# Kernel optimization log

Measured on AMD Instinct MI355X. Metric: run time of the kernel, lower is better.

## Reference

```python
import jax, jax.numpy as jnp
import numpy as np

HEADS = 8
GS = 16
C = 512
E = 512
SCALE = (E / HEADS) ** -0.5
PNAMES = ['sa_qkv_w','sa_qkv_b','sa_pa_w','sa_pa_b','sa_ln1_g','sa_ln1_b','sa_f1_w','sa_f1_b','sa_f2_w','sa_f2_b','sa_ln2_g','sa_ln2_b','sa_c1_w','sa_c1_b','sa_c2_w','sa_c2_b','sa_bn_g','sa_bn_b','ca_q_w','ca_q_b','ca_k_w','ca_k_b','ca_v_w','ca_v_b','ca_pa_w','ca_pa_b','p_q_w','p_q_b','p_k_w','p_k_b','p_v_w','p_v_b','p_pa_w','p_pa_b','p_ln_g','p_ln_b','p_lin_w','p_lin_b']


def _ln(x, g, b, eps=1e-5):
    m = x.mean(-1, keepdims=True)
    v = jnp.var(x, axis=-1, keepdims=True)
    return (x - m) / jnp.sqrt(v + eps) * g + b


def _conv1x1(x, w, b):
    return jnp.einsum('bchw,oc->bohw', x, w) + b[None, :, None, None]


def _up_ac(x, out=GS):
    # bilinear upsample, align_corners=True (nn.UpsamplingBilinear2d)
    H = x.shape[2]
    pos = jnp.arange(out) * (H - 1) / (out - 1)
    lo = jnp.floor(pos).astype(jnp.int32)
    hi = jnp.minimum(lo + 1, H - 1)
    w = (pos - lo).astype(x.dtype)
    xr = x[:, :, lo, :] * (1 - w)[None, None, :, None] + x[:, :, hi, :] * w[None, None, :, None]
    return xr[:, :, :, lo] * (1 - w) + xr[:, :, :, hi] * w


def _asri(x, p):
    # Sequence_ASRI: GAP tokens -> attention over the batch axis -> pixel-shuffle back
    B = x.shape[0]; ch = E // HEADS
    gap = x.mean((2, 3))                                             # [B,C]
    qkv = (gap @ p['sa_qkv_w'].T + p['sa_qkv_b']).reshape(B, 4, ch, HEADS).transpose(1, 3, 0, 2)  # [4,H,B,ch]
    q, k, v, skip = qkv[0], qkv[1], qkv[2], qkv[3]
    attn = jax.nn.softmax(jnp.einsum('hbc,hdc->hbd', q, k) * SCALE, -1)  # [H,B,B]
    o = jnp.einsum('hbd,hdc->hbc', attn, v)
    merge = lambda t: t.transpose(1, 2, 0).reshape(B, E)             # 'head b c -> b (c head)'
    a = merge(o) @ p['sa_pa_w'].T + p['sa_pa_b'] + merge(skip)
    h = jax.nn.relu(_ln(a, p['sa_ln1_g'], p['sa_ln1_b']) @ p['sa_f1_w'].T + p['sa_f1_b'])
    a = h @ p['sa_f2_w'].T + p['sa_f2_b'] + a
    s = _ln(a, p['sa_ln2_g'], p['sa_ln2_b']) @ p['sa_c1_w'].T + p['sa_c1_b']  # [B,C*16]
    s = _up_ac(s.reshape(B, C, 4, 4))                                 # pixel shuffle p1=p2=4 then bilinear to 16x16
    s = _conv1x1(s, p['sa_c2_w'], p['sa_c2_b'])
    # BatchNorm2d in eval mode (running_mean=0, running_var=1, eps=1e-5)
    s = s / np.float32(np.sqrt(1.0 + 1e-5)) * p['sa_bn_g'][None, :, None, None] + p['sa_bn_b'][None, :, None, None]
    return x + jax.nn.relu(s)


def _sscm(x1, x2, p):
    # Sequence_SSCM: GAP-token q/k over batch axis, full spatial v
    B = x1.shape[0]; ch = E // HEADS
    q = (x1.mean((2, 3)) @ p['ca_q_w'].T + p['ca_q_b']).reshape(B, ch, HEADS).transpose(2, 0, 1)  # [H,B,ch]
    k = (x2.mean((2, 3)) @ p['ca_k_w'].T + p['ca_k_b']).reshape(B, ch, HEADS).transpose(2, 0, 1)
    v = _conv1x1(x2, p['ca_v_w'], p['ca_v_b']).reshape(B, ch, HEADS, GS, GS).transpose(2, 0, 1, 3, 4).reshape(HEADS, B, ch * GS * GS)
    attn = jax.nn.softmax(jnp.einsum('hbc,hdc->hbd', q, k) * SCALE, -1)  # [H,B,B]
    o = jnp.einsum('hbd,hdm->hbm', attn, v)
    o = o.reshape(HEADS, B, ch, GS, GS).transpose(1, 2, 0, 3, 4).reshape(B, E, GS, GS)
    return jax.nn.relu(_conv1x1(o, p['ca_pa_w'], p['ca_pa_b']))


def _pixel(x1, x2, p):
    # Pixel_SSCM: pixel-wise cross-batch attention (no scale -- matches source)
    B = x1.shape[0]; ch = E // HEADS; N = GS * GS
    split = lambda t: t.reshape(B, ch, HEADS, N).transpose(2, 0, 3, 1)   # 'b (c head) h w -> head b (h w) c'
    q = split(_conv1x1(x1, p['p_q_w'], p['p_q_b']))                      # [H,B,N,ch]
    k = split(_conv1x1(x2, p['p_k_w'], p['p_k_b']))
    v = split(_conv1x1(x2, p['p_v_w'], p['p_v_b'])).reshape(HEADS, B * N, ch)
    attn = jax.nn.softmax(jnp.einsum('hbnc,hqmc->hbqnm', q, k), -1)      # [H,B,B,N,N]
    attn = attn.transpose(1, 0, 3, 2, 4).reshape(B, HEADS, N, B * N)     # 'head b q h w -> b head h (q w)'
    o = jnp.einsum('bhnm,hmc->bhnc', attn, v)
    o = o.transpose(0, 3, 1, 2).reshape(B, E, GS, GS)                    # 'b head (h w) c -> b (c head) h w'
    o = _conv1x1(o, p['p_pa_w'], p['p_pa_b']) + x1
    t = o.reshape(B, C, N).transpose(0, 2, 1)                            # [B,N,C]
    t = jax.nn.relu(_ln(t, p['p_ln_g'], p['p_ln_b']) @ p['p_lin_w'].T + p['p_lin_b'])
    return t.transpose(0, 2, 1).reshape(B, C, GS, GS)


def _hrlm(p, xs, xq):
    sa_s = _asri(xs, p)
    sa_q = _asri(xq, p)
    ca_s = _sscm(sa_s, sa_q, p)
    ca_q = _sscm(sa_q, sa_s, p)
    return _pixel(sa_s, ca_q, p), _pixel(sa_q, ca_s, p)


def setup_inputs():
    key = jax.random.key(0)
    ks = iter(jax.random.split(key, 64))
    w = lambda *s: (jax.random.normal(next(ks), s) * 0.02).astype(jnp.float32)
    z = lambda n: jnp.zeros((n,), jnp.float32)
    o = lambda n: jnp.ones((n,), jnp.float32)
    return dict(
        fea_support=jax.random.normal(next(ks), (8, C, GS, GS), jnp.float32),
        fea_query=jax.random.normal(next(ks), (8, C, GS, GS), jnp.float32),
        sa_qkv_w=w(4 * E, C), sa_qkv_b=z(4 * E),
        sa_pa_w=w(E, E), sa_pa_b=z(E),
        sa_ln1_g=o(E), sa_ln1_b=z(E),
        sa_f1_w=w(E, E), sa_f1_b=z(E), sa_f2_w=w(E, E), sa_f2_b=z(E),
        sa_ln2_g=o(E), sa_ln2_b=z(E),
        sa_c1_w=w(C * 16, E), sa_c1_b=z(C * 16),
        sa_c2_w=w(C, E), sa_c2_b=z(C),
        sa_bn_g=o(C), sa_bn_b=z(C),
        ca_q_w=w(E, C), ca_q_b=z(E), ca_k_w=w(E, C), ca_k_b=z(E),
        ca_v_w=w(E, C), ca_v_b=z(E), ca_pa_w=w(C, E), ca_pa_b=z(C),
        p_q_w=w(E, C), p_q_b=z(E), p_k_w=w(E, C), p_k_b=z(E),
        p_v_w=w(E, C), p_v_b=z(E), p_pa_w=w(C, E), p_pa_b=z(C),
        p_ln_g=o(C), p_ln_b=z(C), p_lin_w=w(C, C), p_lin_b=z(C),
    )


def reference(fea_support, fea_query, sa_qkv_w, sa_qkv_b, sa_pa_w, sa_pa_b, sa_ln1_g, sa_ln1_b, sa_f1_w, sa_f1_b, sa_f2_w, sa_f2_b, sa_ln2_g, sa_ln2_b, sa_c1_w, sa_c1_b, sa_c2_w, sa_c2_b, sa_bn_g, sa_bn_b, ca_q_w, ca_q_b, ca_k_w, ca_k_b, ca_v_w, ca_v_b, ca_pa_w, ca_pa_b, p_q_w, p_q_b, p_k_w, p_k_b, p_v_w, p_v_b, p_pa_w, p_pa_b, p_ln_g, p_ln_b, p_lin_w, p_lin_b):
    p = dict(zip(PNAMES, (sa_qkv_w, sa_qkv_b, sa_pa_w, sa_pa_b, sa_ln1_g, sa_ln1_b, sa_f1_w, sa_f1_b, sa_f2_w, sa_f2_b, sa_ln2_g, sa_ln2_b, sa_c1_w, sa_c1_b, sa_c2_w, sa_c2_b, sa_bn_g, sa_bn_b, ca_q_w, ca_q_b, ca_k_w, ca_k_b, ca_v_w, ca_v_b, ca_pa_w, ca_pa_b, p_q_w, p_q_b, p_k_w, p_k_b, p_v_w, p_v_b, p_pa_w, p_pa_b, p_ln_g, p_ln_b, p_lin_w, p_lin_b)))
    return _hrlm(p, fea_support, fea_query)
```

## Files before the change

### kernel.cpp

```cpp
#include <hip/hip_runtime.h>
#include <cmath>

#define IMG 131072
#define BIGF 1048576

#define CF_RELU  1
#define CF_RES   2
#define CF_BN    4
#define CF_SPLIT 8
#define CF_TRANS 16

typedef __attribute__((ext_vector_type(8))) short short8;
typedef __attribute__((ext_vector_type(4))) short short4v;
typedef __attribute__((ext_vector_type(4))) float f32x4;

__device__ __forceinline__ float wave_sum(float v){
    #pragma unroll
    for (int off = 32; off; off >>= 1) v += __shfl_xor(v, off);
    return v;
}

__device__ __forceinline__ unsigned short bf16_rn(float x){
    union { float f; unsigned u; } v; v.f = x;
    unsigned r = v.u + 0x7FFF + ((v.u >> 16) & 1);
    return (unsigned short)(r >> 16);
}
__device__ __forceinline__ float bf16_to_f(unsigned short h){
    union { float f; unsigned u; } v; v.u = ((unsigned)h) << 16;
    return v.f;
}
__device__ __forceinline__ unsigned pk_hi(unsigned a, unsigned b){
    return __builtin_amdgcn_perm(b, a, 0x05040100u);
}
__device__ __forceinline__ unsigned pk_lo(unsigned a, unsigned b){
    return __builtin_amdgcn_perm(b, a, 0x07060302u);
}

struct GapJobs  { const float* x[2]; float* o[2]; };
struct G8Job    { const float* in; const float* W; const float* bias; const float* add; float* out; };
struct G8Jobs   { G8Job j[4]; };
struct AAJobs   { const float* qkv[2]; float* om[2]; };
struct LnJobs   { const float* in[2]; float* out[2]; };
struct UpJobs   { const float* in[2]; float* out[2]; };
struct SAJobs   { const float* q8[2]; const float* k8[2]; float* aw[2]; };
struct SPJobs   { const float* aw[2]; const float* v[2]; float* out[2]; };
struct ZJobs    { float* p[2]; };
struct ConvJob  { const float* X; const float* W; const float* B; const float* R;
                  const float* bng; const float* bnb; float* O; int flags; };
struct ConvJobs { ConvJob j[6]; };
struct PixJob   { const unsigned* Q; const unsigned* K; const unsigned* V; float* O; };
struct PixJobs  { PixJob j[2]; };

__global__ __launch_bounds__(64) void k_gap(GapJobs jo){
    const int br = blockIdx.y;
    const int bc = blockIdx.x;
    const int lane = threadIdx.x;
    const float* p = jo.x[br] + (size_t)bc * 256;
    float s = p[lane] + p[lane + 64] + p[lane + 128] + p[lane + 192];
    s = wave_sum(s);
    if (lane == 0) jo.o[br][bc] = s * (1.0f / 256.0f);
}

__global__ __launch_bounds__(64) void k_gemm8(G8Jobs jo, int add_off, int add_stride, int O, int relu){
    const G8Job j = jo.j[blockIdx.y];
    const int o = blockIdx.x;
    const int lane = threadIdx.x;
    const float* wr = j.W + (size_t)o * 512;
    float acc[8] = {0,0,0,0,0,0,0,0};
    #pragma unroll
    for (int i = 0; i < 8; i++){
        float w = wr[lane + 64*i];
        #pragma unroll
        for (int b = 0; b < 8; b++) acc[b] += w * j.in[b*512 + lane + 64*i];
// ... 61 lines not shown
}

__global__ __launch_bounds__(256) void k_up(UpJobs jo){
    const int br = blockIdx.y;
    const int idx = blockIdx.x*256 + threadIdx.x;
    const int x = idx & 15, y = (idx >> 4) & 15, bc = idx >> 8;
    float px = (float)(x*3) / 15.0f, py = (float)(y*3) / 15.0f;
    int lx = (int)px, ly = (int)py;
    float wx = px - lx, wy = py - ly;
    int hx = min(lx+1, 3), hy = min(ly+1, 3);
    const float* p = jo.in[br] + (size_t)bc * 16;
    float v00 = p[ly*4+lx], v01 = p[ly*4+hx], v10 = p[hy*4+lx], v11 = p[hy*4+hx];
    float a0 = v00*(1.f-wy) + v10*wy;
    float a1 = v01*(1.f-wy) + v11*wy;
    jo.out[br][idx] = a0*(1.f-wx) + a1*wx;
}

__global__ __launch_bounds__(256) void k_zero(ZJobs jo){
    jo.p[blockIdx.y][(size_t)blockIdx.x*256 + threadIdx.x] = 0.f;
}

#define LDK 40
__device__ __forceinline__ void convm_body(
    const float* __restrict__ Xb, const float* __restrict__ W,
    const float* __restrict__ bias, const float* __restrict__ resb,
    const float* __restrict__ bng, const float* __restrict__ bnb, float bninv,
    float* __restrict__ outb, int flags, int o0, int n0, unsigned short* lds)
{
    const int tid512 = threadIdx.x;
    const int g   = tid512 >> 8;
    const int tid = tid512 & 255;
    unsigned short* sAh = lds + g*10240;
    unsigned short* sAl = sAh + 2560;
    unsigned short* sBh = sAl + 2560;
    unsigned short* sBl = sBh + 2560;
    const int wv = tid >> 6, lane = tid & 63;
    const int quad = lane >> 4, l16 = lane & 15;
    const int wo = (wv >> 1) * 32, wn = (wv & 1) * 32;
    const int so  = tid >> 2, sk8 = (tid & 3) * 8;
    const int sp  = tid & 15, sn  = (tid >> 4) * 4;

    const bool trans = (flags & CF_TRANS) != 0;
    int so_g = o0 + so;
    if (trans) so_g = ((so_g & 63) << 3) | (so_g >> 6);

    const float* wrow = W + (size_t)so_g*512 + g*256 + sk8;
    const float* xrow = Xb + (size_t)(g*256 + 2*sp)*256 + n0 + sn;

    f32x4 acc[2][2] = {};
    float4 a0 = *(const float4*)(wrow);
    float4 a1 = *(const float4*)(wrow + 4);
    float4 x0 = *(const float4*)(xrow);
    float4 x1 = *(const float4*)(xrow + 256);

    for (int k0 = 0; k0 < 256; k0 += 32){
        __syncthreads();
        {
            float wa[8] = {a0.x,a0.y,a0.z,a0.w,a1.x,a1.y,a1.z,a1.w};
            #pragma unroll
            for (int j = 0; j < 4; j++){
                unsigned short h0 = bf16_rn(wa[2*j]);
                unsigned short h1 = bf16_rn(wa[2*j+1]);
                unsigned short g0 = bf16_rn(wa[2*j]   - bf16_to_f(h0));
                unsigned short g1 = bf16_rn(wa[2*j+1] - bf16_to_f(h1));
                *(unsigned*)&sAh[so*LDK + sk8 + 2*j] = (unsigned)h0 | ((unsigned)h1 << 16);
                *(unsigned*)&sAl[so*LDK + sk8 + 2*j] = (unsigned)g0 | ((unsigned)g1 << 16);
            }
            float xe[4] = {x0.x,x0.y,x0.z,x0.w};
            float xo[4] = {x1.x,x1.y,x1.z,x1.w};
            #pragma unroll
            for (int j = 0; j < 4; j++){
                unsigned short h0 = bf16_rn(xe[j]);
                unsigned short h1 = bf16_rn(xo[j]);
                unsigned short g0 = bf16_rn(xe[j] - bf16_to_f(h0));
                unsigned short g1 = bf16_rn(xo[j] - bf16_to_f(h1));
                *(unsigned*)&sBh[(sn+j)*LDK + 2*sp] = (unsigned)h0 | ((unsigned)h1 << 16);
                *(unsigned*)&sBl[(sn+j)*LDK + 2*sp] = (unsigned)g0 | ((unsigned)g1 << 16);
            }
        }
        __syncthreads();
        if (k0 + 32 < 256){
            a0 = *(const float4*)(wrow + k0 + 32);
            a1 = *(const float4*)(wrow + k0 + 36);
            x0 = *(const float4*)(xrow + (size_t)(k0+32)*256);
            x1 = *(const float4*)(xrow + (size_t)(k0+32)*256 + 256);
        }
        short8 ah[2], al[2], bh[2], bl[2];
        #pragma unroll
        for (int t = 0; t < 2; t++){
            int ai = (wo + 16*t + l16)*LDK + quad*8;
            ah[t] = *(const short8*)&sAh[ai];
            al[t] = *(const short8*)&sAl[ai];
            int bi = (wn + 16*t + l16)*LDK + quad*8;
            bh[t] = *(const short8*)&sBh[bi];
            bl[t] = *(const short8*)&sBl[bi];
        }
        if (trans){
            #pragma unroll
            for (int mt = 0; mt < 2; mt++){
                #pragma unroll
                for (int nt = 0; nt < 2; nt++){
                    acc[mt][nt] = __builtin_amdgcn_mfma_f32_16x16x32_bf16(bh[nt], ah[mt], acc[mt][nt], 0, 0, 0);
                    acc[mt][nt] = __builtin_amdgcn_mfma_f32_16x16x32_bf16(bl[nt], ah[mt], acc[mt][nt], 0, 0, 0);
                    acc[mt][nt] = __builtin_amdgcn_mfma_f32_16x16x32_bf16(bh[nt], al[mt], acc[mt][nt], 0, 0, 0);
                }
            }
        } else {
            #pragma unroll
// ... 20 lines not shown
    __syncthreads();
    if (g == 0){
        float* r = red + tid*20;
        #pragma unroll
        for (int mt = 0; mt < 2; mt++)
            #pragma unroll
            for (int nt = 0; nt < 2; nt++){
                f32x4 o4 = *(const f32x4*)(r + (mt*2+nt)*4);
                acc[mt][nt] += o4;
            }
        if (trans){
            unsigned* op = (unsigned*)outb;
            #pragma unroll
            for (int mt = 0; mt < 2; mt++){
                #pragma unroll
                for (int nt = 0; nt < 2; nt++){
                    const int p  = o0 + wo + 16*mt + l16;
                    const int nb = n0 + wn + 16*nt + quad*4;
                    const int osrc = ((p & 63) << 3) | (p >> 6);
                    const float bs = bias[osrc];
                    #pragma unroll
                    for (int rr = 0; rr < 4; rr++){
                        float v = acc[mt][nt][rr] + bs;
                        unsigned short hi = bf16_rn(v);
                        unsigned short lo = bf16_rn(v - bf16_to_f(hi));
                        op[(size_t)(nb+rr)*512 + p] = (unsigned)hi | ((unsigned)lo << 16);
                    }
                }
            }
        } else {
            #pragma unroll
            for (int mt = 0; mt < 2; mt++){
                #pragma unroll
                for (int nt = 0; nt < 2; nt++){
                    const int n  = n0 + wn + 16*nt + l16;
                    const int ob = o0 + wo + 16*mt + quad*4;
                    #pragma unroll
                    for (int rr = 0; rr < 4; rr++){
                        const int o = ob + rr;
                        float v = acc[mt][nt][rr] + bias[o];
                        if (flags & CF_BN)   v = v*(bninv*bng[o]) + bnb[o];
                        if (flags & CF_RELU) v = fmaxf(v, 0.f);
                        if (flags & CF_RES)  v += resb[(size_t)o*256 + n];
                        if (flags & CF_SPLIT){
                            unsigned short hi = bf16_rn(v);
                            unsigned short lo = bf16_rn(v - bf16_to_f(hi));
                            unsigned pk = (unsigned)hi | ((unsigned)lo << 16);
                            ((unsigned*)outb)[(size_t)o*256 + n] = pk;
                        } else {
                            outb[(size_t)o*256 + n] = v;
                        }
                    }
                }
            }
        }
    }
}

__global__ __launch_bounds__(512) void k_convm(ConvJobs jo, float bninv)
{
    __shared__ unsigned short lds[20480];
    const int z = blockIdx.z;
    const ConvJob j = jo.j[z >> 3];
    const int b = z & 7;
    convm_body(j.X + (size_t)b*IMG, j.W, j.B, j.R ? j.R + (size_t)b*IMG : nullptr,
               j.bng, j.bnb, bninv, j.O + (size_t)b*IMG, j.flags,
               blockIdx.y*64, blockIdx.x*64, lds);
}

__global__ __launch_bounds__(64) void k_sscm_attn(SAJobs jo)
{
    const int br = blockIdx.y;
    const int h = blockIdx.x >> 3, b = blockIdx.x & 7, c = threadIdx.x;
    const int ci = c*8 + h;
    float qc = jo.q8[br][b*512 + ci];
    float s[8];
    #pragma unroll
    for (int d = 0; d < 8; d++){
        float p = qc * jo.k8[br][d*512 + ci];
        p = wave_sum(p);
        s[d] = p * 0.125f;
    }
    float m = s[0];
    #pragma unroll
    for (int d = 1; d < 8; d++) m = fmaxf(m, s[d]);
    float sum = 0.f;
    #pragma unroll
    for (int d = 0; d < 8; d++){ s[d] = __expf(s[d]-m); sum += s[d]; }
    float r = 1.f/sum;
// ... 12 lines not shown
    const int pix = idx & 255, e = (idx >> 8) & 511, b = idx >> 17;
    const int h = e & 7;
    const float* aw = jo.aw[br] + (h*8 + b)*8;
    const float* v = jo.v[br];
    float acc = 0.f;
    #pragma unroll
    for (int d = 0; d < 8; d++) acc += aw[d] * v[(size_t)d*IMG + (size_t)e*256 + pix];
    jo.out[br][idx] = acc;
}

__global__ __launch_bounds__(256) void k_pixel_mfma(PixJobs jo)
{
    __shared__ char smem[40960];
    unsigned short* sQh = (unsigned short*)smem;
    unsigned short* sQl = sQh + 2*64*40;
    unsigned short* sKh = sQl + 2*64*40;
    unsigned short* sKl = sKh + 2*64*40;
    unsigned short* sP  = (unsigned short*)smem;
    unsigned short* sVh = sKh;
    unsigned short* sVl = sKl;

    const int br = blockIdx.y >> 3, b = blockIdx.y & 7;
    const PixJob J = jo.j[br];
    const int nt = blockIdx.x & 3, d = blockIdx.x >> 2;
    const int h = blockIdx.z;
    const int tid = threadIdx.x;
    const int wv = tid >> 6, lane = tid & 63;
    const int quad = lane >> 4, l16 = lane & 15;
    const int n0 = nt * 64;

    {
        const unsigned* Qt = J.Q + (size_t)b*IMG + (size_t)n0*512 + h*64;
        const int q = tid >> 2, i0 = (tid & 3) * 16;
        const unsigned* src = Qt + (size_t)q*512 + i0;
        uint4 w0 = *(const uint4*)(src);
        uint4 w1 = *(const uint4*)(src + 4);
        uint4 w2 = *(const uint4*)(src + 8);
        uint4 w3 = *(const uint4*)(src + 12);
        unsigned hb[8], lb[8];
        hb[0]=pk_hi(w0.x,w0.y); hb[1]=pk_hi(w0.z,w0.w); hb[2]=pk_hi(w1.x,w1.y); hb[3]=pk_hi(w1.z,w1.w);
        hb[4]=pk_hi(w2.x,w2.y); hb[5]=pk_hi(w2.z,w2.w); hb[6]=pk_hi(w3.x,w3.y); hb[7]=pk_hi(w3.z,w3.w);
        lb[0]=pk_lo(w0.x,w0.y); lb[1]=pk_lo(w0.z,w0.w); lb[2]=pk_lo(w1.x,w1.y); lb[3]=pk_lo(w1.z,w1.w);
        lb[4]=pk_lo(w2.x,w2.y); lb[5]=pk_lo(w2.z,w2.w); lb[6]=pk_lo(w3.x,w3.y); lb[7]=pk_lo(w3.z,w3.w);
        int dst = (i0>>5)*2560 + q*40 + (i0&31);
        *(uint4*)&sQh[dst]     = *(uint4*)&hb[0];
        *(uint4*)&sQh[dst + 8] = *(uint4*)&hb[4];
        *(uint4*)&sQl[dst]     = *(uint4*)&lb[0];
        *(uint4*)&sQl[dst + 8] = *(uint4*)&lb[4];
    }
    __syncthreads();

    short8 bqh[2], bql[2];
    #pragma unroll
    for (int ks = 0; ks < 2; ks++){
        int idx = ks*2560 + (wv*16 + l16)*40 + quad*8;
        bqh[ks] = *(const short8*)&sQh[idx];
        bql[ks] = *(const short8*)&sQl[idx];
    }

    f32x4 S[16] = {};
    #pragma unroll
    for (int mq = 0; mq < 4; mq++){
        if (mq) __syncthreads();
        {
            const unsigned* Kt = J.K + (size_t)d*IMG + (size_t)(mq*64)*512 + h*64;
            const int mloc = tid & 63, cb0 = tid >> 6;
            #pragma unroll
            for (int p = 0; p < 2; p++){
                int cb = cb0 + 4*p;
                const unsigned* src = Kt + (size_t)mloc*512 + cb*8;
                uint4 wa = *(const uint4*)(src);
                uint4 wb = *(const uint4*)(src + 4);
                union { short8 s; unsigned u[4]; } hu, lu;
                hu.u[0]=pk_hi(wa.x,wa.y); hu.u[1]=pk_hi(wa.z,wa.w);
                hu.u[2]=pk_hi(wb.x,wb.y); hu.u[3]=pk_hi(wb.z,wb.w);
                lu.u[0]=pk_lo(wa.x,wa.y); lu.u[1]=pk_lo(wa.z,wa.w);
                lu.u[2]=pk_lo(wb.x,wb.y); lu.u[3]=pk_lo(wb.z,wb.w);
                int idx = (cb>>2)*2560 + mloc*40 + (cb&3)*8;
                *(short8*)&sKh[idx] = hu.s;
                *(short8*)&sKl[idx] = lu.s;
            }
        }
        __syncthreads();
        #pragma unroll
        for (int mtl = 0; mtl < 4; mtl++){
            int t = mq*4 + mtl;
            #pragma unroll
            for (int ks = 0; ks < 2; ks++){
                int idx = ks*2560 + (mtl*16 + l16)*40 + quad*8;
                short8 ah = *(const short8*)&sKh[idx];
                short8 al = *(const short8*)&sKl[idx];
                S[t] = __builtin_amdgcn_mfma_f32_16x16x32_bf16(ah, bqh[ks], S[t], 0, 0, 0);
                S[t] = __builtin_amdgcn_mfma_f32_16x16x32_bf16(ah, bql[ks], S[t], 0, 0, 0);
                S[t] = __builtin_amdgcn_mfma_f32_16x16x32_bf16(al, bqh[ks], S[t], 0, 0, 0);
            }
        }
    }

    {
        float mx = -3.4e38f;
        #pragma unroll
        for (int t = 0; t < 16; t++)
            #pragma unroll
            for (int r = 0; r < 4; r++) mx = fmaxf(mx, S[t][r]);
        mx = fmaxf(mx, __shfl_xor(mx, 16));
        mx = fmaxf(mx, __shfl_xor(mx, 32));
        float sum = 0.f;
        #pragma unroll
        for (int t = 0; t < 16; t++)
            #pragma unroll
            for (int r = 0; r < 4; r++){ S[t][r] = __expf(S[t][r]-mx); sum += S[t][r]; }
        sum += __shfl_xor(sum, 16);
        sum += __shfl_xor(sum, 32);
        float rr = 1.f/sum;
        #pragma unroll
        for (int t = 0; t < 16; t++)
            #pragma unroll
            for (int r = 0; r < 4; r++) S[t][r] *= rr;
    }

    f32x4 oac[4] = {};
    #pragma unroll
    for (int hm = 0; hm < 2; hm++){
        __syncthreads();
        #pragma unroll
        for (int mtl = 0; mtl < 8; mtl++){
            int t = hm*8 + mtl;
            short4v p4;
            #pragma unroll
            for (int r = 0; r < 4; r++) p4[r] = (short)bf16_rn(S[t][r]);
            int idx = (mtl>>1)*2560 + (wv*16 + l16)*40 + 16*(mtl&1) + quad*4;
            *(short4v*)&sP[idx] = p4;
        }
        #pragma unroll
        for (int sub = 0; sub < 2; sub++){
            if (sub) __syncthreads();
            {
                const unsigned* Vp = J.V + (size_t)d*IMG + (size_t)h*256 + hm*128 + sub*64;
                const int mp = tid & 31, c0 = tid >> 5;
                #pragma unroll
                for (int p = 0; p < 8; p++){
                    int c = c0 + 8*p;
                    const unsigned* src = Vp + (size_t)c*2048 + 2*mp;
                    uint2 w = *(const uint2*)(src);
                    int idx = ((2*mp)>>5)*2560 + c*40 + ((2*mp)&31);
                    *(unsigned*)&sVh[idx] = pk_hi(w.x, w.y);
                    *(unsigned*)&sVl[idx] = pk_lo(w.x, w.y);
                }
            }
            __syncthreads();
            #pragma unroll
            for (int l = 0; l < 2; l++){
                int gks = sub*2 + l;
                int pidx = gks*2560 + (wv*16 + l16)*40 + quad*8;
                short8 bp = *(const short8*)&sP[pidx];
                #pragma unroll
                for (int ct = 0; ct < 4; ct++){
                    int vidx = l*2560 + (ct*16 + l16)*40 + quad*8;
                    short8 vh = *(const short8*)&sVh[vidx];
                    short8 vl = *(const short8*)&sVl[vidx];
                    oac[ct] = __builtin_amdgcn_mfma_f32_16x16x32_bf16(vh, bp, oac[ct], 0, 0, 0);
                    oac[ct] = __builtin_amdgcn_mfma_f32_16x16x32_bf16(vl, bp, oac[ct], 0, 0, 0);
                }
            }
        }
    }

    {
        float* Ob = J.O + (size_t)b * IMG;
        const int q = n0 + wv*16 + l16;
        #pragma unroll
        for (int ct = 0; ct < 4; ct++){
            #pragma unroll
            for (int r = 0; r < 4; r++){
                int c = ct*16 + quad*4 + r;
                unsafeAtomicAdd(&Ob[(size_t)(c*8+h)*256 + q], oac[ct][r]);
            }
        }
    }
}

__global__ __launch_bounds__(64) void k_ln_pix(LnJobs jo,
    const float* __restrict__ g, const float* __restrict__ be)
{
    const int br = blockIdx.y;
    const int bn = blockIdx.x;
    const int b = bn >> 8, n = bn & 255;
    const int lane = threadIdx.x;
    const float* p = jo.in[br] + (size_t)b*IMG + n;
    float v[8]; float s = 0.f;
    #pragma unroll
    for (int i = 0; i < 8; i++){ v[i] = p[(size_t)(lane + 64*i)*256]; s += v[i]; }
    s = wave_sum(s);
    float mean = s * (1.f/512.f);
    float q = 0.f;
    #pragma unroll
    for (int i = 0; i < 8; i++){ float d = v[i]-mean; q += d*d; }
    q = wave_sum(q);
    float rstd = rsqrtf(q*(1.f/512.f) + 1e-5f);
// ... 13 lines not shown
    const float* qkvw  = (const float*)d_in[2];  const float* qkvb = (const float*)d_in[3];
    const float* paw   = (const float*)d_in[4];  const float* pab  = (const float*)d_in[5];
    const float* ln1g  = (const float*)d_in[6];  const float* ln1b = (const float*)d_in[7];
    const float* f1w   = (const float*)d_in[8];  const float* f1b  = (const float*)d_in[9];
    const float* f2w   = (const float*)d_in[10]; const float* f2b  = (const float*)d_in[11];
    const float* ln2g  = (const float*)d_in[12]; const float* ln2b = (const float*)d_in[13];
    const float* c1w   = (const float*)d_in[14]; const float* c1b  = (const float*)d_in[15];
    const float* c2w   = (const float*)d_in[16]; const float* c2b  = (const float*)d_in[17];
    const float* bng   = (const float*)d_in[18]; const float* bnb  = (const float*)d_in[19];
    const float* caqw  = (const float*)d_in[20]; const float* caqb = (const float*)d_in[21];
    const float* cakw  = (const float*)d_in[22]; const float* cakb = (const float*)d_in[23];
    const float* cavw  = (const float*)d_in[24]; const float* cavb = (const float*)d_in[25];
    const float* capw  = (const float*)d_in[26]; const float* capb = (const float*)d_in[27];
    const float* pqw   = (const float*)d_in[28]; const float* pqb  = (const float*)d_in[29];
    const float* pkw   = (const float*)d_in[30]; const float* pkb  = (const float*)d_in[31];
    const float* pvw   = (const float*)d_in[32]; const float* pvb  = (const float*)d_in[33];
    const float* ppw   = (const float*)d_in[34]; const float* ppb  = (const float*)d_in[35];
    const float* plng  = (const float*)d_in[36]; const float* plnb = (const float*)d_in[37];
    const float* plinw = (const float*)d_in[38]; const float* plinb= (const float*)d_in[39];

    const size_t SMF = 262144;
    float* ws = (float*)d_ws;
    float* smb = ws;
    float* B[12];
    for (int i = 0; i < 12; i++) B[i] = ws + SMF + (size_t)i*BIGF;
    float* sa_s = B[0]; float* sa_q = B[1];
    float* ca_s = B[2]; float* ca_q = B[3];
    const bool paired_pixel = ws_size >= (SMF + 12*(size_t)BIGF)*sizeof(float) + 1024;

    auto SM = [&](int br){ return smb + (size_t)br*131072; };
    auto GAP=[&](int br){ return SM(br); };            auto QKV=[&](int br){ return SM(br)+4096; };
    auto OM =[&](int br){ return SM(br)+20480; };      auto AA =[&](int br){ return SM(br)+24576; };
    auto HB =[&](int br){ return SM(br)+28672; };      auto A2 =[&](int br){ return SM(br)+32768; };
    auto LNB=[&](int br){ return SM(br)+36864; };      auto S8 =[&](int br){ return SM(br)+40960; };
    auto ATW=[&](int br){ return SM(br)+106496; };     auto Q8 =[&](int br){ return SM(br)+107008; };
    auto K8 =[&](int br){ return SM(br)+111104; };

    const float bninv = 1.0f / sqrtf(1.0f + 1e-5f);
    float* out0 = (float*)d_out;
    float* out1 = out0 + (size_t)BIGF;

    {
        GapJobs gj = {{xs, xq}, {GAP(0), GAP(1)}};
        k_gap<<<dim3(4096,2), 64, 0, stream>>>(gj);
        G8Jobs qj = {{{GAP(0), qkvw, qkvb, nullptr, QKV(0)}, {GAP(1), qkvw, qkvb, nullptr, QKV(1)}}};
        k_gemm8<<<dim3(2048,2), 64, 0, stream>>>(qj, 0, 0, 2048, 0);
        AAJobs aj = {{QKV(0), QKV(1)}, {OM(0), OM(1)}};
        k_asri_attn<<<dim3(64,2), 64, 0, stream>>>(aj);
        G8Jobs pj = {{{OM(0), paw, pab, QKV(0), AA(0)}, {OM(1), paw, pab, QKV(1), AA(1)}}};
        k_gemm8<<<dim3(512,2), 64, 0, stream>>>(pj, 1536, 2048, 512, 0);
        LnJobs l1 = {{AA(0), AA(1)}, {LNB(0), LNB(1)}};
        k_ln8<<<dim3(8,2), 64, 0, stream>>>(l1, ln1g, ln1b);
        G8Jobs fj = {{{LNB(0), f1w, f1b, nullptr, HB(0)}, {LNB(1), f1w, f1b, nullptr, HB(1)}}};
        k_gemm8<<<dim3(512,2), 64, 0, stream>>>(fj, 0, 0, 512, 1);
        G8Jobs f2j = {{{HB(0), f2w, f2b, AA(0), A2(0)}, {HB(1), f2w, f2b, AA(1), A2(1)}}};
        k_gemm8<<<dim3(512,2), 64, 0, stream>>>(f2j, 0, 512, 512, 0);
        LnJobs l2 = {{A2(0), A2(1)}, {LNB(0), LNB(1)}};
        k_ln8<<<dim3(8,2), 64, 0, stream>>>(l2, ln2g, ln2b);
        G8Jobs cj = {{{LNB(0), c1w, c1b, nullptr, S8(0)}, {LNB(1), c1w, c1b, nullptr, S8(1)}}};
        k_gemm8<<<dim3(8192,2), 64, 0, stream>>>(cj, 0, 0, 8192, 0);
        UpJobs uj = {{S8(0), S8(1)}, {B[4], B[5]}};
        k_up<<<dim3(4096,2), 256, 0, stream>>>(uj);
        ConvJobs c2j = {};
        c2j.j[0] = {B[4], c2w, c2b, xs, bng, bnb, sa_s, CF_BN|CF_RELU|CF_RES};
        c2j.j[1] = {B[5], c2w, c2b, xq, bng, bnb, sa_q, CF_BN|CF_RELU|CF_RES};
        k_convm<<<dim3(4,8,16), 512, 0, stream>>>(c2j, bninv);
    }

    {
        GapJobs gj = {{sa_s, sa_q}, {GAP(0), GAP(1)}};
        k_gap<<<dim3(4096,2), 64, 0, stream>>>(gj);
        G8Jobs qj = {{{GAP(0), caqw, caqb, nullptr, Q8(0)},
                      {GAP(1), cakw, cakb, nullptr, K8(0)},
                      {GAP(1), caqw, caqb, nullptr, Q8(1)},
                      {GAP(0), cakw, cakb, nullptr, K8(1)}}};
        k_gemm8<<<dim3(512,4), 64, 0, stream>>>(qj, 0, 0, 512, 0);
        SAJobs sj = {{Q8(0), Q8(1)}, {K8(0), K8(1)}, {ATW(0), ATW(1)}};
        k_sscm_attn<<<dim3(64,2), 64, 0, stream>>>(sj);
        ConvJobs vj = {};
        vj.j[0] = {sa_q, cavw, cavb, nullptr, nullptr, nullptr, B[4], 0};
        vj.j[1] = {sa_s, cavw, cavb, nullptr, nullptr, nullptr, B[5], 0};
        k_convm<<<dim3(4,8,16), 512, 0, stream>>>(vj, 1.f);
        SPJobs pj = {{ATW(0), ATW(1)}, {B[4], B[5]}, {B[6], B[7]}};
        k_sscm_apply<<<dim3(4096,2), 256, 0, stream>>>(pj);
        ConvJobs aj = {};
        aj.j[0] = {B[6], capw, capb, nullptr, nullptr, nullptr, ca_s, CF_RELU};
        aj.j[1] = {B[7], capw, capb, nullptr, nullptr, nullptr, ca_q, CF_RELU};
        k_convm<<<dim3(4,8,16), 512, 0, stream>>>(aj, 1.f);
    }

    if (paired_pixel){
        ConvJobs qkvj = {};
        qkvj.j[0] = {sa_s, pqw, pqb, nullptr, nullptr, nullptr, B[4],  CF_SPLIT|CF_TRANS};
        qkvj.j[1] = {ca_q, pkw, pkb, nullptr, nullptr, nullptr, B[5],  CF_SPLIT|CF_TRANS};
        qkvj.j[2] = {ca_q, pvw, pvb, nullptr, nullptr, nullptr, B[6],  CF_SPLIT};
        qkvj.j[3] = {sa_q, pqw, pqb, nullptr, nullptr, nullptr, B[8],  CF_SPLIT|CF_TRANS};
        qkvj.j[4] = {ca_s, pkw, pkb, nullptr, nullptr, nullptr, B[9],  CF_SPLIT|CF_TRANS};
        qkvj.j[5] = {ca_s, pvw, pvb, nullptr, nullptr, nullptr, B[10], CF_SPLIT};
        k_convm<<<dim3(4,8,48), 512, 0, stream>>>(qkvj, 1.f);
        ZJobs zj = {{B[7], B[11]}};
        k_zero<<<dim3(4096,2), 256, 0, stream>>>(zj);
        PixJobs pxj = {{{(const unsigned*)B[4], (const unsigned*)B[5], (const unsigned*)B[6], B[7]},
                        {(const unsigned*)B[8], (const unsigned*)B[9], (const unsigned*)B[10], B[11]}}};
        k_pixel_mfma<<<dim3(32,16,8), 256, 0, stream>>>(pxj);
        ConvJobs ppj = {};
        ppj.j[0] = {B[7],  ppw, ppb, sa_s, nullptr, nullptr, out0, CF_RES};
        ppj.j[1] = {B[11], ppw, ppb, sa_q, nullptr, nullptr, out1, CF_RES};
        k_convm<<<dim3(4,8,16), 512, 0, stream>>>(ppj, 1.f);
        LnJobs lj = {{out0, out1}, {B[4], B[8]}};
        k_ln_pix<<<dim3(2048,2), 64, 0, stream>>>(lj, plng, plnb);
        ConvJobs lnj = {};
        lnj.j[0] = {B[4], plinw, plinb, nullptr, nullptr, nullptr, out0, CF_RELU};
        lnj.j[1] = {B[8], plinw, plinb, nullptr, nullptr, nullptr, out1, CF_RELU};
        k_convm<<<dim3(4,8,16), 512, 0, stream>>>(lnj, 1.f);
    } else {
        auto pixel1 = [&](const float* x1, const float* x2, float* out){
            ConvJobs qkvj = {};
            qkvj.j[0] = {x1, pqw, pqb, nullptr, nullptr, nullptr, B[4], CF_SPLIT|CF_TRANS};
            qkvj.j[1] = {x2, pkw, pkb, nullptr, nullptr, nullptr, B[5], CF_SPLIT|CF_TRANS};
            qkvj.j[2] = {x2, pvw, pvb, nullptr, nullptr, nullptr, B[6], CF_SPLIT};
            k_convm<<<dim3(4,8,24), 512, 0, stream>>>(qkvj, 1.f);
            ZJobs zj = {{B[7], B[7]}};
            k_zero<<<dim3(4096,1), 256, 0, stream>>>(zj);
            PixJobs pxj = {{{(const unsigned*)B[4], (const unsigned*)B[5], (const unsigned*)B[6], B[7]},
                            {(const unsigned*)B[4], (const unsigned*)B[5], (const unsigned*)B[6], B[7]}}};
            k_pixel_mfma<<<dim3(32,8,8), 256, 0, stream>>>(pxj);
            ConvJobs ppj = {};
            ppj.j[0] = {B[7], ppw, ppb, x1, nullptr, nullptr, out, CF_RES};
            k_convm<<<dim3(4,8,8), 512, 0, stream>>>(ppj, 1.f);
            LnJobs lj = {{out, out}, {B[4], B[4]}};
            k_ln_pix<<<dim3(2048,1), 64, 0, stream>>>(lj, plng, plnb);
            ConvJobs lnj = {};
            lnj.j[0] = {B[4], plinw, plinb, nullptr, nullptr, nullptr, out, CF_RELU};
            k_convm<<<dim3(4,8,8), 512, 0, stream>>>(lnj, 1.f);
        };
        pixel1(sa_s, ca_q, out0);
        pixel1(sa_q, ca_s, out1);
    }

    (void)in_sizes; (void)n_in; (void)out_size;
}
```

Baseline: 473.6 us.

## Accumulate pixel attention over d groups in registers; replace atomics with split buffers

The pixel attention kernel now loops over 4 batch-axis keys (d) per block and accumulates their outputs in registers, cutting the grid from 32 to 8 blocks in x. When enough workspace exists, the two d-groups are written with plain stores to two separate buffers instead of atomically added into a zeroed buffer, so the zero kernel is skipped. The output projection conv sums the two buffers on load through a new second-input pointer. This trades fewer atomics and one fewer launch for fewer, longer-running blocks and a dependency on larger workspace.

```diff
diff --git a/kernel.cpp b/kernel.cpp
--- a/kernel.cpp
+++ b/kernel.cpp
@@ -28,6 +28,11 @@
 __device__ __forceinline__ float bf16_to_f(unsigned short h){
     union { float f; unsigned u; } v; v.u = ((unsigned)h) << 16;
     return v.f;
+}
+__device__ __forceinline__ unsigned pack_split(float x){
+    unsigned short hi = bf16_rn(x);
+    unsigned short lo = bf16_rn(x - bf16_to_f(hi));
+    return (unsigned)hi | ((unsigned)lo << 16);
 }
 __device__ __forceinline__ unsigned pk_hi(unsigned a, unsigned b){
     return __builtin_amdgcn_perm(b, a, 0x05040100u);
@@ -45,10 +50,10 @@
 struct SAJobs   { const float* q8[2]; const float* k8[2]; float* aw[2]; };
 struct SPJobs   { const float* aw[2]; const float* v[2]; float* out[2]; };
 struct ZJobs    { float* p[2]; };
-struct ConvJob  { const float* X; const float* W; const float* B; const float* R;
+struct ConvJob  { const float* X; const float* X2; const float* W; const float* B; const float* R;
                   const float* bng; const float* bnb; float* O; int flags; };
 struct ConvJobs { ConvJob j[6]; };
-struct PixJob   { const unsigned* Q; const unsigned* K; const unsigned* V; float* O; };
+struct PixJob   { const unsigned* Q; const unsigned* K; const unsigned* V; float* Oa; float* Ob; };
 struct PixJobs  { PixJob j[2]; };
 
 __global__ __launch_bounds__(64) void k_gap(GapJobs jo){
@@ -156,7 +161,8 @@
 
 #define LDK 40
 __device__ __forceinline__ void convm_body(
-    const float* __restrict__ Xb, const float* __restrict__ W,
+    const float* __restrict__ Xb, const float* __restrict__ X2b,
+    const float* __restrict__ W,
     const float* __restrict__ bias, const float* __restrict__ resb,
     const float* __restrict__ bng, const float* __restrict__ bnb, float bninv,
     float* __restrict__ outb, int flags, int o0, int n0, unsigned short* lds)
@@ -179,13 +185,24 @@
     if (trans) so_g = ((so_g & 63) << 3) | (so_g >> 6);
 
     const float* wrow = W + (size_t)so_g*512 + g*256 + sk8;
-    const float* xrow = Xb + (size_t)(g*256 + 2*sp)*256 + n0 + sn;
+    const size_t xoff = (size_t)(g*256 + 2*sp)*256 + n0 + sn;
+    const float* xrow  = Xb + xoff;
+    const float* x2row = X2b ? X2b + xoff : nullptr;
+
+    auto ldx4 = [&](size_t off){
+        float4 v = *(const float4*)(xrow + off);
+        if (x2row){
+            float4 w2 = *(const float4*)(x2row + off);
+            v.x += w2.x; v.y += w2.y; v.z += w2.z; v.w += w2.w;
+        }
+        return v;
+    };
 
     f32x4 acc[2][2] = {};
     float4 a0 = *(const float4*)(wrow);
     float4 a1 = *(const float4*)(wrow + 4);
-    float4 x0 = *(const float4*)(xrow);
-    float4 x1 = *(const float4*)(xrow + 256);
+    float4 x0 = ldx4(0);
+    float4 x1 = ldx4(256);
 
     for (int k0 = 0; k0 < 256; k0 += 32){
         __syncthreads();
@@ -216,8 +233,8 @@
         if (k0 + 32 < 256){
             a0 = *(const float4*)(wrow + k0 + 32);
             a1 = *(const float4*)(wrow + k0 + 36);
-            x0 = *(const float4*)(xrow + (size_t)(k0+32)*256);
-            x1 = *(const float4*)(xrow + (size_t)(k0+32)*256 + 256);
+            x0 = ldx4((size_t)(k0+32)*256);
+            x1 = ldx4((size_t)(k0+32)*256 + 256);
         }
         short8 ah[2], al[2], bh[2], bl[2];
         #pragma unroll
@@ -284,9 +301,7 @@
                     #pragma unroll
                     for (int rr = 0; rr < 4; rr++){
                         float v = acc[mt][nt][rr] + bs;
-                        unsigned short hi = bf16_rn(v);
-                        unsigned short lo = bf16_rn(v - bf16_to_f(hi));
-                        op[(size_t)(nb+rr)*512 + p] = (unsigned)hi | ((unsigned)lo << 16);
+                        op[(size_t)(nb+rr)*512 + p] = pack_split(v);
                     }
                 }
             }
@@ -305,10 +320,7 @@
                         if (flags & CF_RELU) v = fmaxf(v, 0.f);
                         if (flags & CF_RES)  v += resb[(size_t)o*256 + n];
                         if (flags & CF_SPLIT){
-                            unsigned short hi = bf16_rn(v);
-                            unsigned short lo = bf16_rn(v - bf16_to_f(hi));
-                            unsigned pk = (unsigned)hi | ((unsigned)lo << 16);
-                            ((unsigned*)outb)[(size_t)o*256 + n] = pk;
+                            ((unsigned*)outb)[(size_t)o*256 + n] = pack_split(v);
                         } else {
                             outb[(size_t)o*256 + n] = v;
                         }
@@ -325,8 +337,12 @@
     const int z = blockIdx.z;
     const ConvJob j = jo.j[z >> 3];
     const int b = z & 7;
-    convm_body(j.X + (size_t)b*IMG, j.W, j.B, j.R ? j.R + (size_t)b*IMG : nullptr,
-               j.bng, j.bnb, bninv, j.O + (size_t)b*IMG, j.flags,
+    convm_body(j.X + (size_t)b*IMG,
+               j.X2 ? j.X2 + (size_t)b*IMG : nullptr,
+               j.W, j.B,
+               j.R ? j.R + (size_t)b*IMG : nullptr,
+               j.bng, j.bnb, bninv,
+               j.O + (size_t)b*IMG, j.flags,
                blockIdx.y*64, blockIdx.x*64, lds);
 }
 
@@ -385,7 +401,7 @@
 
     const int br = blockIdx.y >> 3, b = blockIdx.y & 7;
     const PixJob J = jo.j[br];
-    const int nt = blockIdx.x & 3, d = blockIdx.x >> 2;
+    const int nt = blockIdx.x & 3, dg = blockIdx.x >> 2;
     const int h = blockIdx.z;
     const int tid = threadIdx.x;
     const int wv = tid >> 6, lane = tid & 63;
@@ -421,123 +437,140 @@
         bql[ks] = *(const short8*)&sQl[idx];
     }
 
-    f32x4 S[16] = {};
-    #pragma unroll
-    for (int mq = 0; mq < 4; mq++){
-        if (mq) __syncthreads();
+    f32x4 oac[4] = {};
+
+    for (int dd = 0; dd < 4; dd++){
+        const int d = dg*4 + dd;
+
+        f32x4 S[16] = {};
+        #pragma unroll
+        for (int mq = 0; mq < 4; mq++){
+            if (mq | dd) __syncthreads();
+            {
+                const unsigned* Kt = J.K + (size_t)d*IMG + (size_t)(mq*64)*512 + h*64;
+                const int mloc = tid & 63, cb0 = tid >> 6;
+                #pragma unroll
+                for (int p = 0; p < 2; p++){
+                    int cb = cb0 + 4*p;
+                    const unsigned* src = Kt + (size_t)mloc*512 + cb*8;
+                    uint4 wa = *(const uint4*)(src);
+                    uint4 wb = *(const uint4*)(src + 4);
+                    union { short8 s; unsigned u[4]; } hu, lu;
+                    hu.u[0]=pk_hi(wa.x,wa.y); hu.u[1]=pk_hi(wa.z,wa.w);
+                    hu.u[2]=pk_hi(wb.x,wb.y); hu.u[3]=pk_hi(wb.z,wb.w);
+                    lu.u[0]=pk_lo(wa.x,wa.y); lu.u[1]=pk_lo(wa.z,wa.w);
+                    lu.u[2]=pk_lo(wb.x,wb.y); lu.u[3]=pk_lo(wb.z,wb.w);
+                    int idx = (cb>>2)*2560 + mloc*40 + (cb&3)*8;
+                    *(short8*)&sKh[idx] = hu.s;
+                    *(short8*)&sKl[idx] = lu.s;
+                }
+            }
+            __syncthreads();
+            #pragma unroll
+            for (int mtl = 0; mtl < 4; mtl++){
+                int t = mq*4 + mtl;
+                #pragma unroll
+                for (int ks = 0; ks < 2; ks++){
+                    int idx = ks*2560 + (mtl*16 + l16)*40 + quad*8;
+                    short8 ah = *(const short8*)&sKh[idx];
+                    short8 al = *(const short8*)&sKl[idx];
+                    S[t] = __builtin_amdgcn_mfma_f32_16x16x32_bf16(ah, bqh[ks], S[t], 0, 0, 0);
+                    S[t] = __builtin_amdgcn_mfma_f32_16x16x32_bf16(ah, bql[ks], S[t], 0, 0, 0);
+                    S[t] = __builtin_amdgcn_mfma_f32_16x16x32_bf16(al, bqh[ks], S[t], 0, 0, 0);
+                }
+            }
+        }
+
         {
-            const unsigned* Kt = J.K + (size_t)d*IMG + (size_t)(mq*64)*512 + h*64;
-            const int mloc = tid & 63, cb0 = tid >> 6;
-            #pragma unroll
-            for (int p = 0; p < 2; p++){
-                int cb = cb0 + 4*p;
-                const unsigned* src = Kt + (size_t)mloc*512 + cb*8;
-                uint4 wa = *(const uint4*)(src);
-                uint4 wb = *(const uint4*)(src + 4);
-                union { short8 s; unsigned u[4]; } hu, lu;
-                hu.u[0]=pk_hi(wa.x,wa.y); hu.u[1]=pk_hi(wa.z,wa.w);
-                hu.u[2]=pk_hi(wb.x,wb.y); hu.u[3]=pk_hi(wb.z,wb.w);
-                lu.u[0]=pk_lo(wa.x,wa.y); lu.u[1]=pk_lo(wa.z,wa.w);
-                lu.u[2]=pk_lo(wb.x,wb.y); lu.u[3]=pk_lo(wb.z,wb.w);
-                int idx = (cb>>2)*2560 + mloc*40 + (cb&3)*8;
-                *(short8*)&sKh[idx] = hu.s;
-                *(short8*)&sKl[idx] = lu.s;
-            }
-        }
-        __syncthreads();
+            float mx = -3.4e38f;
+            #pragma unroll
+            for (int t = 0; t < 16; t++)
+                #pragma unroll
+                for (int r = 0; r < 4; r++) mx = fmaxf(mx, S[t][r]);
+            mx = fmaxf(mx, __shfl_xor(mx, 16));
+            mx = fmaxf(mx, __shfl_xor(mx, 32));
+            float sum = 0.f;
+            #pragma unroll
+            for (int t = 0; t < 16; t++)
+                #pragma unroll
+                for (int r = 0; r < 4; r++){ S[t][r] = __expf(S[t][r]-mx); sum += S[t][r]; }
+            sum += __shfl_xor(sum, 16);
+            sum += __shfl_xor(sum, 32);
+            float rr = 1.f/sum;
+            #pragma unroll
+            for (int t = 0; t < 16; t++)
+                #pragma unroll
+                for (int r = 0; r < 4; r++) S[t][r] *= rr;
+        }
+
         #pragma unroll
-        for (int mtl = 0; mtl < 4; mtl++){
-            int t = mq*4 + mtl;
-            #pragma unroll
-            for (int ks = 0; ks < 2; ks++){
-                int idx = ks*2560 + (mtl*16 + l16)*40 + quad*8;
-                short8 ah = *(const short8*)&sKh[idx];
-                short8 al = *(const short8*)&sKl[idx];
-                S[t] = __builtin_amdgcn_mfma_f32_16x16x32_bf16(ah, bqh[ks], S[t], 0, 0, 0);
-                S[t] = __builtin_amdgcn_mfma_f32_16x16x32_bf16(ah, bql[ks], S[t], 0, 0, 0);
-                S[t] = __builtin_amdgcn_mfma_f32_16x16x32_bf16(al, bqh[ks], S[t], 0, 0, 0);
+        for (int hm = 0; hm < 2; hm++){
+            __syncthreads();
+            #pragma unroll
+            for (int mtl = 0; mtl < 8; mtl++){
+                int t = hm*8 + mtl;
+                short4v p4;
+                #pragma unroll
+                for (int r = 0; r < 4; r++) p4[r] = (short)bf16_rn(S[t][r]);
+                int idx = (mtl>>1)*2560 + (wv*16 + l16)*40 + 16*(mtl&1) + quad*4;
+                *(short4v*)&sP[idx] = p4;
+            }
+            #pragma unroll
+            for (int sub = 0; sub < 2; sub++){
+                if (sub) __syncthreads();
+                {
+                    const unsigned* Vp = J.V + (size_t)d*IMG + (size_t)h*256 + hm*128 + sub*64;
+                    const int mp = tid & 31, c0 = tid >> 5;
+                    #pragma unroll
+                    for (int p = 0; p < 8; p++){
+                        int c = c0 + 8*p;
+                        const unsigned* src = Vp + (size_t)c*2048 + 2*mp;
+                        uint2 w = *(const uint2*)(src);
+                        int idx = ((2*mp)>>5)*2560 + c*40 + ((2*mp)&31);
+                        *(unsigned*)&sVh[idx] = pk_hi(w.x, w.y);
+                        *(unsigned*)&sVl[idx] = pk_lo(w.x, w.y);
+                    }
+                }
+                __syncthreads();
+                #pragma unroll
+                for (int l = 0; l < 2; l++){
+                    int gks = sub*2 + l;
+                    int pidx = gks*2560 + (wv*16 + l16)*40 + quad*8;
+                    short8 bp = *(const short8*)&sP[pidx];
+                    #pragma unroll
+                    for (int ct = 0; ct < 4; ct++){
+                        int vidx = l*2560 + (ct*16 + l16)*40 + quad*8;
+                        short8 vh = *(const short8*)&sVh[vidx];
+                        short8 vl = *(const short8*)&sVl[vidx];
+                        oac[ct] = __builtin_amdgcn_mfma_f32_16x16x32_bf16(vh, bp, oac[ct], 0, 0, 0);
+                        oac[ct] = __builtin_amdgcn_mfma_f32_16x16x32_bf16(vl, bp, oac[ct], 0, 0, 0);
+                    }
+                }
             }
         }
     }
 
     {
-        float mx = -3.4e38f;
-        #pragma unroll
-        for (int t = 0; t < 16; t++)
-            #pragma unroll
-            for (int r = 0; r < 4; r++) mx = fmaxf(mx, S[t][r]);
-        mx = fmaxf(mx, __shfl_xor(mx, 16));
-        mx = fmaxf(mx, __shfl_xor(mx, 32));
-        float sum = 0.f;
-        #pragma unroll
-        for (int t = 0; t < 16; t++)
-            #pragma unroll
-            for (int r = 0; r < 4; r++){ S[t][r] = __expf(S[t][r]-mx); sum += S[t][r]; }
-        sum += __shfl_xor(sum, 16);
-        sum += __shfl_xor(sum, 32);
-        float rr = 1.f/sum;
-        #pragma unroll
-        for (int t = 0; t < 16; t++)
-            #pragma unroll
-            for (int r = 0; r < 4; r++) S[t][r] *= rr;
-    }
-
-    f32x4 oac[4] = {};
-    #pragma unroll
-    for (int hm = 0; hm < 2; hm++){
-        __syncthreads();
-        #pragma unroll
-        for (int mtl = 0; mtl < 8; mtl++){
-            int t = hm*8 + mtl;
-            short4v p4;
-            #pragma unroll
-            for (int r = 0; r < 4; r++) p4[r] = (short)bf16_rn(S[t][r]);
-            int idx = (mtl>>1)*2560 + (wv*16 + l16)*40 + 16*(mtl&1) + quad*4;
-            *(short4v*)&sP[idx] = p4;
-        }
-        #pragma unroll
-        for (int sub = 0; sub < 2; sub++){
-            if (sub) __syncthreads();
-            {
-                const unsigned* Vp = J.V + (size_t)d*IMG + (size_t)h*256 + hm*128 + sub*64;
-                const int mp = tid & 31, c0 = tid >> 5;
-                #pragma unroll
-                for (int p = 0; p < 8; p++){
-                    int c = c0 + 8*p;
-                    const unsigned* src = Vp + (size_t)c*2048 + 2*mp;
-                    uint2 w = *(const uint2*)(src);
-                    int idx = ((2*mp)>>5)*2560 + c*40 + ((2*mp)&31);
-                    *(unsigned*)&sVh[idx] = pk_hi(w.x, w.y);
-                    *(unsigned*)&sVl[idx] = pk_lo(w.x, w.y);
-                }
-            }
-            __syncthreads();
-            #pragma unroll
-            for (int l = 0; l < 2; l++){
-                int gks = sub*2 + l;
-                int pidx = gks*2560 + (wv*16 + l16)*40 + quad*8;
-                short8 bp = *(const short8*)&sP[pidx];
-                #pragma unroll
-                for (int ct = 0; ct < 4; ct++){
-                    int vidx = l*2560 + (ct*16 + l16)*40 + quad*8;
-                    short8 vh = *(const short8*)&sVh[vidx];
-                    short8 vl = *(const short8*)&sVl[vidx];
-                    oac[ct] = __builtin_amdgcn_mfma_f32_16x16x32_bf16(vh, bp, oac[ct], 0, 0, 0);
-                    oac[ct] = __builtin_amdgcn_mfma_f32_16x16x32_bf16(vl, bp, oac[ct], 0, 0, 0);
-                }
-            }
-        }
-    }
-
-    {
-        float* Ob = J.O + (size_t)b * IMG;
+        float* base = (J.Ob ? (dg ? J.Ob : J.Oa) : J.Oa);
+        float* Obp = base + (size_t)b * IMG;
         const int q = n0 + wv*16 + l16;
-        #pragma unroll
-        for (int ct = 0; ct < 4; ct++){
-            #pragma unroll
-            for (int r = 0; r < 4; r++){
-                int c = ct*16 + quad*4 + r;
-                unsafeAtomicAdd(&Ob[(size_t)(c*8+h)*256 + q], oac[ct][r]);
+        if (J.Ob){
+            #pragma unroll
+            for (int ct = 0; ct < 4; ct++){
+                #pragma unroll
+                for (int r = 0; r < 4; r++){
+                    int c = ct*16 + quad*4 + r;
+                    Obp[(size_t)(c*8+h)*256 + q] = oac[ct][r];
+                }
+            }
+        } else {
+            #pragma unroll
+            for (int ct = 0; ct < 4; ct++){
+                #pragma unroll
+                for (int r = 0; r < 4; r++){
+                    int c = ct*16 + quad*4 + r;
+                    unsafeAtomicAdd(&Obp[(size_t)(c*8+h)*256 + q], oac[ct][r]);
+                }
             }
         }
     }
@@ -597,11 +630,12 @@
     const size_t SMF = 262144;
     float* ws = (float*)d_ws;
     float* smb = ws;
-    float* B[12];
-    for (int i = 0; i < 12; i++) B[i] = ws + SMF + (size_t)i*BIGF;
+    float* B[14];
+    for (int i = 0; i < 14; i++) B[i] = ws + SMF + (size_t)i*BIGF;
     float* sa_s = B[0]; float* sa_q = B[1];
     float* ca_s = B[2]; float* ca_q = B[3];
     const bool paired_pixel = ws_size >= (SMF + 12*(size_t)BIGF)*sizeof(float) + 1024;
+    const bool has_dsplit   = ws_size >= (SMF + 14*(size_t)BIGF)*sizeof(float) + 1024;
 
     auto SM = [&](int br){ return smb + (size_t)br*131072; };
     auto GAP=[&](int br){ return SM(br); };            auto QKV=[&](int br){ return SM(br)+4096; };
@@ -637,8 +671,8 @@
         UpJobs uj = {{S8(0), S8(1)}, {B[4], B[5]}};
         k_up<<<dim3(4096,2), 256, 0, stream>>>(uj);
         ConvJobs c2j = {};
-        c2j.j[0] = {B[4], c2w, c2b, xs, bng, bnb, sa_s, CF_BN|CF_RELU|CF_RES};
-        c2j.j[1] = {B[5], c2w, c2b, xq, bng, bnb, sa_q, CF_BN|CF_RELU|CF_RES};
+        c2j.j[0] = {B[4], nullptr, c2w, c2b, xs, bng, bnb, sa_s, CF_BN|CF_RELU|CF_RES};
+        c2j.j[1] = {B[5], nullptr, c2w, c2b, xq, bng, bnb, sa_q, CF_BN|CF_RELU|CF_RES};
         k_convm<<<dim3(4,8,16), 512, 0, stream>>>(c2j, bninv);
     }
 
@@ -653,60 +687,64 @@
         SAJobs sj = {{Q8(0), Q8(1)}, {K8(0), K8(1)}, {ATW(0), ATW(1)}};
         k_sscm_attn<<<dim3(64,2), 64, 0, stream>>>(sj);
         ConvJobs vj = {};
-        vj.j[0] = {sa_q, cavw, cavb, nullptr, nullptr, nullptr, B[4], 0};
-        vj.j[1] = {sa_s, cavw, cavb, nullptr, nullptr, nullptr, B[5], 0};
+        vj.j[0] = {sa_q, nullptr, cavw, cavb, nullptr, nullptr, nullptr, B[4], 0};
+        vj.j[1] = {sa_s, nullptr, cavw, cavb, nullptr, nullptr, nullptr, B[5], 0};
         k_convm<<<dim3(4,8,16), 512, 0, stream>>>(vj, 1.f);
         SPJobs pj = {{ATW(0), ATW(1)}, {B[4], B[5]}, {B[6], B[7]}};
         k_sscm_apply<<<dim3(4096,2), 256, 0, stream>>>(pj);
         ConvJobs aj = {};
-        aj.j[0] = {B[6], capw, capb, nullptr, nullptr, nullptr, ca_s, CF_RELU};
-        aj.j[1] = {B[7], capw, capb, nullptr, nullptr, nullptr, ca_q, CF_RELU};
+        aj.j[0] = {B[6], nullptr, capw, capb, nullptr, nullptr, nullptr, ca_s, CF_RELU};
+        aj.j[1] = {B[7], nullptr, capw, capb, nullptr, nullptr, nullptr, ca_q, CF_RELU};
         k_convm<<<dim3(4,8,16), 512, 0, stream>>>(aj, 1.f);
     }
 
     if (paired_pixel){
         ConvJobs qkvj = {};
-        qkvj.j[0] = {sa_s, pqw, pqb, nullptr, nullptr, nullptr, B[4],  CF_SPLIT|CF_TRANS};
-        qkvj.j[1] = {ca_q, pkw, pkb, nullptr, nullptr, nullptr, B[5],  CF_SPLIT|CF_TRANS};
-        qkvj.j[2] = {ca_q, pvw, pvb, nullptr, nullptr, nullptr, B[6],  CF_SPLIT};
-        qkvj.j[3] = {sa_q, pqw, pqb, nullptr, nullptr, nullptr, B[8],  CF_SPLIT|CF_TRANS};
-        qkvj.j[4] = {ca_s, pkw, pkb, nullptr, nullptr, nullptr, B[9],  CF_SPLIT|CF_TRANS};
-        qkvj.j[5] = {ca_s, pvw, pvb, nullptr, nullptr, nullptr, B[10], CF_SPLIT};
+        qkvj.j[0] = {sa_s, nullptr, pqw, pqb, nullptr, nullptr, nullptr, B[4],  CF_SPLIT|CF_TRANS};
+        qkvj.j[1] = {ca_q, nullptr, pkw, pkb, nullptr, nullptr, nullptr, B[5],  CF_SPLIT|CF_TRANS};
+        qkvj.j[2] = {ca_q, nullptr, pvw, pvb, nullptr, nullptr, nullptr, B[6],  CF_SPLIT};
+        qkvj.j[3] = {sa_q, nullptr, pqw, pqb, nullptr, nullptr, nullptr, B[8],  CF_SPLIT|CF_TRANS};
+        qkvj.j[4] = {ca_s, nullptr, pkw, pkb, nullptr, nullptr, nullptr, B[9],  CF_SPLIT|CF_TRANS};
+        qkvj.j[5] = {ca_s, nullptr, pvw, pvb, nullptr, nullptr, nullptr, B[10], CF_SPLIT};
         k_convm<<<dim3(4,8,48), 512, 0, stream>>>(qkvj, 1.f);
-        ZJobs zj = {{B[7], B[11]}};
-        k_zero<<<dim3(4096,2), 256, 0, stream>>>(zj);
-        PixJobs pxj = {{{(const unsigned*)B[4], (const unsigned*)B[5], (const unsigned*)B[6], B[7]},
-                        {(const unsigned*)B[8], (const unsigned*)B[9], (const unsigned*)B[10], B[11]}}};
-        k_pixel_mfma<<<dim3(32,16,8), 256, 0, stream>>>(pxj);
+        if (!has_dsplit){
+            ZJobs zj = {{B[7], B[11]}};
+            k_zero<<<dim3(4096,2), 256, 0, stream>>>(zj);
+        }
+        float* o2a = has_dsplit ? B[12] : nullptr;
+        float* o2b = has_dsplit ? B[13] : nullptr;
+        PixJobs pxj = {{{(const unsigned*)B[4], (const unsigned*)B[5], (const unsigned*)B[6],  B[7],  o2a},
+                        {(const unsigned*)B[8], (const unsigned*)B[9], (const unsigned*)B[10], B[11], o2b}}};
+        k_pixel_mfma<<<dim3(8,16,8), 256, 0, stream>>>(pxj);
         ConvJobs ppj = {};
-        ppj.j[0] = {B[7],  ppw, ppb, sa_s, nullptr, nullptr, out0, CF_RES};
-        ppj.j[1] = {B[11], ppw, ppb, sa_q, nullptr, nullptr, out1, CF_RES};
+        ppj.j[0] = {B[7],  o2a, ppw, ppb, sa_s, nullptr, nullptr, out0, CF_RES};
+        ppj.j[1] = {B[11], o2b, ppw, ppb, sa_q, nullptr, nullptr, out1, CF_RES};
         k_convm<<<dim3(4,8,16), 512, 0, stream>>>(ppj, 1.f);
         LnJobs lj = {{out0, out1}, {B[4], B[8]}};
         k_ln_pix<<<dim3(2048,2), 64, 0, stream>>>(lj, plng, plnb);
         ConvJobs lnj = {};
-        lnj.j[0] = {B[4], plinw, plinb, nullptr, nullptr, nullptr, out0, CF_RELU};
-        lnj.j[1] = {B[8], plinw, plinb, nullptr, nullptr, nullptr, out1, CF_RELU};
+        lnj.j[0] = {B[4], nullptr, plinw, plinb, nullptr, nullptr, nullptr, out0, CF_RELU};
+        lnj.j[1] = {B[8], nullptr, plinw, plinb, nullptr, nullptr, nullptr, out1, CF_RELU};
         k_convm<<<dim3(4,8,16), 512, 0, stream>>>(lnj, 1.f);
     } else {
         auto pixel1 = [&](const float* x1, const float* x2, float* out){
             ConvJobs qkvj = {};
-            qkvj.j[0] = {x1, pqw, pqb, nullptr, nullptr, nullptr, B[4], CF_SPLIT|CF_TRANS};
-            qkvj.j[1] = {x2, pkw, pkb, nullptr, nullptr, nullptr, B[5], CF_SPLIT|CF_TRANS};
-            qkvj.j[2] = {x2, pvw, pvb, nullptr, nullptr, nullptr, B[6], CF_SPLIT};
+            qkvj.j[0] = {x1, nullptr, pqw, pqb, nullptr, nullptr, nullptr, B[4], CF_SPLIT|CF_TRANS};
+            qkvj.j[1] = {x2, nullptr, pkw, pkb, nullptr, nullptr, nullptr, B[5], CF_SPLIT|CF_TRANS};
+            qkvj.j[2] = {x2, nullptr, pvw, pvb, nullptr, nullptr, nullptr, B[6], CF_SPLIT};
             k_convm<<<dim3(4,8,24), 512, 0, stream>>>(qkvj, 1.f);
             ZJobs zj = {{B[7], B[7]}};
             k_zero<<<dim3(4096,1), 256, 0, stream>>>(zj);
-            PixJobs pxj = {{{(const unsigned*)B[4], (const unsigned*)B[5], (const unsigned*)B[6], B[7]},
-                            {(const unsigned*)B[4], (const unsigned*)B[5], (const unsigned*)B[6], B[7]}}};
-            k_pixel_mfma<<<dim3(32,8,8), 256, 0, stream>>>(pxj);
+            PixJobs pxj = {{{(const unsigned*)B[4], (const unsigned*)B[5], (const unsigned*)B[6], B[7], nullptr},
+                            {(const unsigned*)B[4], (const unsigned*)B[5], (const unsigned*)B[6], B[7], nullptr}}};
+            k_pixel_mfma<<<dim3(8,8,8), 256, 0, stream>>>(pxj);
             ConvJobs ppj = {};
-            ppj.j[0] = {B[7], ppw, ppb, x1, nullptr, nullptr, out, CF_RES};
+            ppj.j[0] = {B[7], nullptr, ppw, ppb, x1, nullptr, nullptr, out, CF_RES};
             k_convm<<<dim3(4,8,8), 512, 0, stream>>>(ppj, 1.f);
             LnJobs lj = {{out, out}, {B[4], B[4]}};
             k_ln_pix<<<dim3(2048,1), 64, 0, stream>>>(lj, plng, plnb);
             ConvJobs lnj = {};
-            lnj.j[0] = {B[4], plinw, plinb, nullptr, nullptr, nullptr, out, CF_RELU};
+            lnj.j[0] = {B[4], nullptr, plinw, plinb, nullptr, nullptr, nullptr, out, CF_RELU};
             k_convm<<<dim3(4,8,8), 512, 0, stream>>>(lnj, 1.f);
         };
         pixel1(sa_s, ca_q, out0);
```

Result: slower. 488.1 us (+3.1%).
